# Optimization experiments

Hardware: AMD Instinct MI355X
Metric: run time of the kernel (lower is better)

Reference implementation:

```python
import jax, jax.numpy as jnp
import numpy as np

N = 20000
NEG_SLOPE = 0.2


def gatv2_layer(x, src, dst, edge_attr, Wl, bl, Wr, br, We, att, bias, H, C):
    """PyG GATv2Conv: add self-loops (edge_attr fill='mean'), gather-score-softmax-aggregate."""
    n = x.shape[0]
    E = src.shape[0]
    # --- add self loops, self-loop edge_attr = mean of incoming edge_attr per node ---
    ea_sum = jax.ops.segment_sum(edge_attr, dst, num_segments=n)
    deg = jax.ops.segment_sum(jnp.ones((E, 1), x.dtype), dst, num_segments=n)
    ea_loop = ea_sum / jnp.maximum(deg, 1.0)
    loop = jnp.arange(n)
    src_a = jnp.concatenate([src, loop])
    dst_a = jnp.concatenate([dst, loop])
    ea = jnp.concatenate([edge_attr, ea_loop], axis=0)
    # --- linear projections ---
    xl = (x @ Wl + bl).reshape(n, H, C)   # source-side features
    xr = (x @ Wr + br).reshape(n, H, C)   # target-side features
    e = (ea @ We).reshape(-1, H, C)       # edge features
    # --- per-edge GATv2 attention score ---
    m = xl[src_a] + xr[dst_a] + e                          # [E', H, C]
    s = jnp.sum(jax.nn.leaky_relu(m, NEG_SLOPE) * att, -1)  # [E', H]
    # --- softmax over incoming edges of each target node ---
    smax = jax.ops.segment_max(s, dst_a, num_segments=n)
    ex = jnp.exp(s - smax[dst_a])
    denom = jax.ops.segment_sum(ex, dst_a, num_segments=n)
    alpha = ex / (denom[dst_a] + 1e-16)                    # [E', H]
    # --- aggregate messages (alpha * x_l[src]) ---
    out = jax.ops.segment_sum(alpha[..., None] * xl[src_a], dst_a, num_segments=n)
    return out.reshape(n, H * C) + bias


def setup_inputs() -> dict:
    key = jax.random.key(0)
    ks = jax.random.split(key, 20)
    F, HID, H1, A = 128, 32, 8, 128
    E = 640000
    d = {}
    d["x"] = jax.random.normal(ks[0], (N, F), jnp.float32)
    d["edge_index"] = jax.random.randint(ks[1], (2, E), 0, N, jnp.int32).astype(jnp.int64)
    d["edge_attr"] = jax.random.normal(ks[2], (E, 1), jnp.float32)
    # layer 1 params (in=F, out=HID, heads=H1)
    d["W1l"] = jax.random.normal(ks[3], (F, H1 * HID), jnp.float32) * 0.05
    d["b1l"] = jnp.zeros((H1 * HID,), jnp.float32)
    d["W1r"] = jax.random.normal(ks[4], (F, H1 * HID), jnp.float32) * 0.05
    d["b1r"] = jnp.zeros((H1 * HID,), jnp.float32)
    d["We1"] = jax.random.normal(ks[5], (1, H1 * HID), jnp.float32) * 0.05
    d["att1"] = jax.random.normal(ks[6], (H1, HID), jnp.float32) * 0.05
    d["bias1"] = jnp.zeros((H1 * HID,), jnp.float32)
    # layer 2 params (in=H1*HID, out=A, heads=1)
    d["W2l"] = jax.random.normal(ks[7], (H1 * HID, A), jnp.float32) * 0.05
    d["b2l"] = jnp.zeros((A,), jnp.float32)
    d["W2r"] = jax.random.normal(ks[8], (H1 * HID, A), jnp.float32) * 0.05
    d["b2r"] = jnp.zeros((A,), jnp.float32)
    d["We2"] = jax.random.normal(ks[9], (1, A), jnp.float32) * 0.05
    d["att2"] = jax.random.normal(ks[10], (1, A), jnp.float32) * 0.05
    d["bias2"] = jnp.zeros((A,), jnp.float32)
    d["alpha"] = jnp.array(0.0, jnp.float32)
    return d


def reference(x, edge_index, edge_attr, W1l, b1l, W1r, b1r, We1, att1, bias1,
              W2l, b2l, W2r, b2r, We2, att2, bias2, alpha):
    src, dst = edge_index[0], edge_index[1]
    h = jax.nn.relu(gatv2_layer(x, src, dst, edge_attr, W1l, b1l, W1r, b1r,
                                We1, att1, bias1, H=8, C=32))
    h = jax.nn.relu(gatv2_layer(h, src, dst, edge_attr, W2l, b2l, W2r, b2r,
                                We2, att2, bias2, H=1, C=128))
    pooled = jnp.mean(h, axis=0, keepdims=True)  # global_mean_pool, single graph -> [1, A]
    return jax.nn.softmax(pooled, axis=1), jax.nn.sigmoid(alpha)
```

## Files before the change

### kernel.cpp

```cpp
#include <hip/hip_runtime.h>
#include <math.h>

#define NEG_SLOPE 0.2f
#define LOG2E 1.4426950408889634f

typedef __attribute__((ext_vector_type(8))) short short8;
typedef __attribute__((ext_vector_type(4))) float f32x4;
typedef __attribute__((ext_vector_type(2))) float v2f;

__device__ __forceinline__ int imin(int a, int b) { return a < b ? a : b; }

__device__ __forceinline__ unsigned int f2bf(float f) {
    unsigned int u = __float_as_uint(f);
    return (u + 0x7fffu + ((u >> 16) & 1u)) >> 16;
}
__device__ __forceinline__ float fast_exp2(float x) {
#if __has_builtin(__builtin_amdgcn_exp2f)
    return __builtin_amdgcn_exp2f(x);
#else
    return exp2f(x);
#endif
}
__device__ __forceinline__ unsigned char f2fp8(float v) {
    return (unsigned char)(__builtin_amdgcn_cvt_pk_fp8_f32(v, v, 0, false) & 0xff);
}
template <int CTRL>
__device__ __forceinline__ float dpp_add(float v) {
    int t = __builtin_amdgcn_update_dpp(0, __float_as_int(v), CTRL, 0xF, 0xF, true);
    return v + __int_as_float(t);
}
__device__ __forceinline__ v2f pk_fma(v2f a, v2f b, v2f c) {
    v2f d;
    asm("v_pk_fma_f32 %0, %1, %2, %3" : "=v"(d) : "v"(a), "v"(b), "v"(c));
    return d;
}
__device__ __forceinline__ v2f pk_add(v2f a, v2f b) {
    v2f d;
    asm("v_pk_add_f32 %0, %1, %2" : "=v"(d) : "v"(a), "v"(b));
    return d;
}

__global__ void fused_prep(const int* __restrict__ ei, const float* __restrict__ ea,
                           unsigned long long* __restrict__ hist, int E,
                           const float* __restrict__ x, unsigned short* __restrict__ xb, int nF4,
                           const float* __restrict__ W1l, const float* __restrict__ W1r,
                           const float* __restrict__ W2l, const float* __restrict__ W2r,
                           const float* __restrict__ b1l, const float* __restrict__ b1r,
                           const float* __restrict__ b2l, const float* __restrict__ b2r,
                           unsigned short* __restrict__ Wt1, unsigned short* __restrict__ Wt2,
                           float* __restrict__ b1cat, float* __restrict__ b2cat,
                           int F, int HC1, int HC2) {
    int i = blockIdx.x * blockDim.x + threadIdx.x;
    if (i < E) {
        int d = ei[E + i];
        long long fx = (long long)__float2int_rn(ea[i] * 65536.0f);
        unsigned long long v = ((unsigned long long)fx << 32) | 1ull;
        atomicAdd(&hist[(size_t)d * 8], v);
        return;
    }
    int j = i - E;
    if (j < nF4) {
        float4 v = ((const float4*)x)[j];
        uint2 r;
        r.x = f2bf(v.x) | (f2bf(v.y) << 16);
        r.y = f2bf(v.z) | (f2bf(v.w) << 16);
        ((uint2*)xb)[j] = r;
        return;
    }
    int k = j - nF4;
    int S1 = F * HC1, S2 = HC1 * HC2;
    if (k < S1) {
        int kk = k / HC1, nn = k - kk * HC1;
        Wt1[(size_t)nn * F + kk] = (unsigned short)f2bf(W1l[k]);
    } else if (k < 2 * S1) {
        int m = k - S1;
        int kk = m / HC1, nn = m - kk * HC1;
        Wt1[(size_t)(HC1 + nn) * F + kk] = (unsigned short)f2bf(W1r[m]);
    } else if (k < 2 * S1 + S2) {
        int m = k - 2 * S1;
        int kk = m / HC2, nn = m - kk * HC2;
        Wt2[(size_t)nn * HC1 + kk] = (unsigned short)f2bf(W2l[m]);
    } else if (k < 2 * S1 + 2 * S2) {
        int m = k - 2 * S1 - S2;
        int kk = m / HC2, nn = m - kk * HC2;
        Wt2[(size_t)(HC2 + nn) * HC1 + kk] = (unsigned short)f2bf(W2r[m]);
    } else if (k < 2 * S1 + 2 * S2 + 2 * HC1) {
        int m = k - 2 * S1 - 2 * S2;
        b1cat[m] = (m < HC1) ? b1l[m] : b1r[m - HC1];
    } else if (k < 2 * S1 + 2 * S2 + 2 * HC1 + 2 * HC2) {
        int m = k - 2 * S1 - 2 * S2 - 2 * HC1;
        b2cat[m] = (m < HC2) ? b2l[m] : b2r[m - HC2];
    }
}

__global__ void scan_a(const unsigned long long* __restrict__ hist, int* __restrict__ bsum, int n) {
    __shared__ int wred[4];
    int base = blockIdx.x * 1024;
    int tid = threadIdx.x;
    int s = 0;
#pragma unroll
    for (int k = 0; k < 4; ++k) {
        int i = base + tid + k * 256;
        if (i < n) s += (int)(hist[(size_t)i * 8] & 0xffffffffull);
    }
#pragma unroll
    for (int off = 32; off > 0; off >>= 1) s += __shfl_xor(s, off, 64);
    if ((tid & 63) == 0) wred[tid >> 6] = s;
    __syncthreads();
    if (tid == 0) bsum[blockIdx.x] = wred[0] + wred[1] + wred[2] + wred[3];
}

__global__ void scan_c(const unsigned long long* __restrict__ hist,
                       const int* __restrict__ bsum, int* __restrict__ row_ptr,
                       int* __restrict__ wptr_pad, float* __restrict__ ea_loop,
                       int n, int B) {
    __shared__ int wtot[4];
    __shared__ int sh_base;
    int tid = threadIdx.x;
    int wid = tid >> 6, lane = tid & 63;
    int i0 = blockIdx.x * 1024 + tid * 4;
    int dcnt[4]; float esum[4];
#pragma unroll
    for (int k = 0; k < 4; ++k) {
        if (i0 + k < n) {
            unsigned long long h = hist[(size_t)(i0 + k) * 8];
            dcnt[k] = (int)(h & 0xffffffffull);
            esum[k] = (float)((int)(h >> 32)) * (1.0f / 65536.0f);
        } else { dcnt[k] = 0; esum[k] = 0.0f; }
    }
    int tsum = dcnt[0] + dcnt[1] + dcnt[2] + dcnt[3];
    int s = tsum;
#pragma unroll
    for (int off = 1; off < 64; off <<= 1) {
        int t = __shfl_up(s, off, 64);
        if (lane >= off) s += t;
    }
    if (lane == 63) wtot[wid] = s;
    if (tid < 64) {
        int v   = (tid < B) ? bsum[tid] : 0;
        int pre = (tid < (int)blockIdx.x) ? v : 0;
        int tot = v;
#pragma unroll
        for (int off = 32; off > 0; off >>= 1) {
            pre += __shfl_xor(pre, off, 64);
            tot += __shfl_xor(tot, off, 64);
        }
        if (tid == 0) {
            sh_base = pre;
            if (blockIdx.x == 0) row_ptr[n] = tot;
        }
    }
    __syncthreads();
    int wpre = 0;
#pragma unroll
    for (int k = 0; k < 4; ++k) if (k < wid) wpre += wtot[k];
    int pre = sh_base + wpre + (s - tsum);
    if (i0 < n) {
        int4 e;
        e.x = pre;
        e.y = pre + dcnt[0];
        e.z = e.y + dcnt[1];
        e.w = e.z + dcnt[2];
        *(int4*)(row_ptr + i0) = e;
        int ev[4] = { e.x, e.y, e.z, e.w };
        float4 el;
        el.x = esum[0] / fmaxf((float)dcnt[0], 1.0f);
        el.y = esum[1] / fmaxf((float)dcnt[1], 1.0f);
        el.z = esum[2] / fmaxf((float)dcnt[2], 1.0f);
        el.w = esum[3] / fmaxf((float)dcnt[3], 1.0f);
        *(float4*)(ea_loop + i0) = el;
#pragma unroll
        for (int k = 0; k < 4; ++k) wptr_pad[(size_t)(i0 + k) * 16] = ev[k];
    }
}

__global__ void edge_scatter(const int* __restrict__ ei, const float* __restrict__ ea,
                             int* __restrict__ wptr_pad, int2* __restrict__ spk, int E) {
    int e = blockIdx.x * blockDim.x + threadIdx.x;
    if (e < E) {
        int d = ei[E + e];
        int pos = atomicAdd(&wptr_pad[(size_t)d * 16], 1);
        spk[pos] = make_int2(ei[e], __float_as_int(ea[e]));
    }
}

template <bool OUT_FP8>
__global__ void __launch_bounds__(256)
gemm_bf16(const unsigned short* __restrict__ A, const unsigned short* __restrict__ Bt,
          const float* __restrict__ bias, void* __restrict__ Cv,
          int M, int N, int K) {
    __shared__ __attribute__((aligned(16))) unsigned short As[64 * 40];
    __shared__ __attribute__((aligned(16))) unsigned short Bs[64 * 40];
    int tid  = threadIdx.x;
    int wave = tid >> 6, lane = tid & 63;
    int m0 = blockIdx.x * 64, n0 = blockIdx.y * 64;
    int row = tid >> 2, kg = (tid & 3) * 8;

    f32x4 acc[4] = {};
    for (int kk = 0; kk < K; kk += 32) {
        int gm = m0 + row;
        uint4 av;
        if (gm < M) av = *(const uint4*)(A + (size_t)gm * K + kk + kg);
        else        av = make_uint4(0, 0, 0, 0);
        *(uint4*)&As[row * 40 + kg] = av;
        uint4 bv = *(const uint4*)(Bt + (size_t)(n0 + row) * K + kk + kg);
        *(uint4*)&Bs[row * 40 + kg] = bv;
        __syncthreads();
        short8 a = *(const short8*)&As[(wave * 16 + (lane & 15)) * 40 + (lane >> 4) * 8];
#pragma unroll
        for (int g = 0; g < 4; ++g) {
            short8 b = *(const short8*)&Bs[(g * 16 + (lane & 15)) * 40 + (lane >> 4) * 8];
            acc[g] = __builtin_amdgcn_mfma_f32_16x16x32_bf16(a, b, acc[g], 0, 0, 0);
        }
        __syncthreads();
    }
#pragma unroll
    for (int g = 0; g < 4; ++g) {
        int col = n0 + g * 16 + (lane & 15);
        float bs = bias[col];
#pragma unroll
        for (int r = 0; r < 4; ++r) {
            int grow = m0 + wave * 16 + (lane >> 4) * 4 + r;
            if (grow < M) {
                float val = acc[g][r] + bs;
                if constexpr (OUT_FP8) {
                    ((unsigned char*)Cv)[(size_t)grow * N + col] = f2fp8(val);
                } else {
                    ((unsigned short*)Cv)[(size_t)grow * N + col] = (unsigned short)f2bf(val);
                }
            }
        }
    }
}

template <int NG>
__device__ __forceinline__ void unp2(uint2 u, v2f* xf) {
    xf[0] = __builtin_amdgcn_cvt_pk_f32_fp8(u.x, false);
    xf[1] = __builtin_amdgcn_cvt_pk_f32_fp8(u.x, true);
    if constexpr (NG == 4) {
        xf[2] = __builtin_amdgcn_cvt_pk_f32_fp8(u.y, false);
        xf[3] = __builtin_amdgcn_cvt_pk_f32_fp8(u.y, true);
    }
}
template <int G>
__device__ __forceinline__ float grp_reduce32(float vs) {
    vs = dpp_add<0xB1>(vs);
    if constexpr (G >= 4)  vs = dpp_add<0x4E>(vs);
    if constexpr (G >= 8)  vs = dpp_add<0x141>(vs);
    if constexpr (G >= 16) vs = dpp_add<0x140>(vs);
    if constexpr (G >= 32) {
        int t = __builtin_amdgcn_ds_swizzle(__float_as_int(vs), 0x401F);
        vs += __int_as_float(t);
    }
    return vs;
}

template <int HC, int STRIDE, int C, int OUT_MODE>
__global__ void __launch_bounds__(256)
gat_agg(const unsigned char* __restrict__ xlr,
        const float* __restrict__ We, const float* __restrict__ att,
        const float* __restrict__ bias,
        const int* __restrict__ row_ptr, const int2* __restrict__ spk,
        const float* __restrict__ ea_loop,
        void* __restrict__ out, int n) {
    constexpr int NV = HC / 32;
    constexpr int NG = NV / 2;
    constexpr int G  = C / NV;
    constexpr int SHIFT = (STRIDE == 512) ? 9 : 8;
    constexpr float K23 = 2.0f / 3.0f;
    int wave = threadIdx.x >> 6;
    int lane = threadIdx.x & 63;
    int node = blockIdx.x * 4 + wave;
    if (node >= n) return;
    unsigned int lo32 = (unsigned int)(lane & 31) * NV;
    int half = lane >> 5;

    auto ldd = [&](unsigned int off) -> uint2 {
        uint2 r;
        if constexpr (NV == 8) r = *(const uint2*)(xlr + off);
        else { r.x = *(const unsigned int*)(xlr + off); r.y = 0u; }
        return r;
    };
    auto gat = [&](int s) -> uint2 {
        return ldd(((unsigned int)s << SHIFT) + lo32);
    };

    v2f xr2[NG], We2[NG], att62[NG], o2[NG];
    unp2<NG>(ldd(((unsigned int)node << SHIFT) + HC + lo32), xr2);
#pragma unroll
    for (int g = 0; g < NG; ++g) {
        We2[g]   = *(const v2f*)(We  + lo32 + 2 * g);
        v2f a    = *(const v2f*)(att + lo32 + 2 * g);
        att62[g] = a * (0.6f * LOG2E);
        o2[g]    = v2f{0.0f, 0.0f};
    }
    float l = 0.0f;

    int start = __builtin_amdgcn_readfirstlane(row_ptr[node]);
    int end   = __builtin_amdgcn_readfirstlane(row_ptr[node + 1]);
    float ea_l = ea_loop[node];

    auto process = [&](uint2 du, float w, bool maskhi) {
        v2f xf[NG];
        unp2<NG>(du, xf);
        v2f w2 = {w, w};
        v2f vs6 = {0.0f, 0.0f};
        float vs4 = 0.0f;
#pragma unroll
        for (int g = 0; g < NG; ++g) {
            v2f t  = pk_fma(w2, We2[g], xr2[g]);
            v2f mm = pk_add(xf[g], t);
            vs6 = pk_fma(att62[g], mm, vs6);
            vs4 = fmaf(fabsf(mm.x), att62[g].x, vs4);
            vs4 = fmaf(fabsf(mm.y), att62[g].y, vs4);
        }
        float vs = fmaf(K23, vs4, vs6.x + vs6.y);
        vs = grp_reduce32<G>(vs);
        float pr = fast_exp2(vs);
        if (maskhi && lane >= 32) pr = 0.0f;
        l += pr;
        v2f pr2 = {pr, pr};
#pragma unroll
        for (int g = 0; g < NG; ++g) o2[g] = pk_fma(xf[g], pr2, o2[g]);
    };

    process(ldd(((unsigned int)node << SHIFT) + lo32), ea_l, true);

    int cnt = end - start;
    int npair = cnt >> 1;
    const int2* pp = spk + start + half;

    if (npair >= 2) {
        int2 sA = pp[0], sB = pp[2];
        uint2 gA = gat(sA.x);
        int p = 0;
        for (; p + 2 < npair; p += 2) {
            uint2 gB = gat(sB.x);
            int2 sC = pp[2 * p + 4];
            process(gA, __int_as_float(sA.y), false);
            uint2 gC = gat(sC.x);
            int2 sD = pp[2 * p + 6];
            process(gB, __int_as_float(sB.y), false);
            sA = sC; sB = sD; gA = gC;
        }
        if (npair - p == 2) {
            uint2 gB = gat(sB.x);
            process(gA, __int_as_float(sA.y), false);
            process(gB, __int_as_float(sB.y), false);
        } else {
            process(gA, __int_as_float(sA.y), false);
        }
    } else if (npair == 1) {
        int2 sA = pp[0];
        process(gat(sA.x), __int_as_float(sA.y), false);
    }
    if (cnt & 1) {
        int2 st = spk[end - 1];
        process(gat(st.x), __int_as_float(st.y), true);
    }

    l += __shfl_xor(l, 32, 64);
#pragma unroll
    for (int g = 0; g < NG; ++g) {
        o2[g].x += __shfl_xor(o2[g].x, 32, 64);
        o2[g].y += __shfl_xor(o2[g].y, 32, 64);
    }
    float inv = 1.0f / (l + 1e-16f);

    if (lane < 32) {
        float v[NV];
#pragma unroll
        for (int g = 0; g < NG; ++g) {
            v2f b = *(const v2f*)(bias + lo32 + 2 * g);
            v[2 * g]     = fmaxf(o2[g].x * inv + b.x, 0.0f);
            v[2 * g + 1] = fmaxf(o2[g].y * inv + b.y, 0.0f);
        }
        if constexpr (OUT_MODE == 0) {
            unsigned short* op = (unsigned short*)out + (size_t)node * HC + lo32;
            if constexpr (NV == 8) {
                uint4 t;
                t.x = f2bf(v[0]) | (f2bf(v[1]) << 16);
                t.y = f2bf(v[2]) | (f2bf(v[3]) << 16);
                t.z = f2bf(v[4]) | (f2bf(v[5]) << 16);
                t.w = f2bf(v[6]) | (f2bf(v[7]) << 16);
                *(uint4*)op = t;
            } else {
                uint2 t;
                t.x = f2bf(v[0]) | (f2bf(v[1]) << 16);
                t.y = f2bf(v[2]) | (f2bf(v[3]) << 16);
                *(uint2*)op = t;
            }
        } else {
            float* pacc = (float*)out + (size_t)(blockIdx.x & 255) * 128 + lo32;
#pragma unroll
            for (int j = 0; j < NV; ++j) atomicAdd(&pacc[j], v[j]);
        }
    }
}

__global__ void __launch_bounds__(1024)
pool_final(const float* __restrict__ partial, int nb,
           const float* __restrict__ alpha_in,
           float* __restrict__ out, int n) {
    __shared__ float acc[8][128];
    __shared__ float red[4];
    int t = threadIdx.x & 127;
    int g = threadIdx.x >> 7;
    float s = 0.0f;
    for (int b = g; b < nb; b += 8) s += partial[b * 128 + t];
    acc[g][t] = s;
    __syncthreads();
    if (threadIdx.x < 128) {
        float tot = 0.0f;
#pragma unroll
        for (int k = 0; k < 8; ++k) tot += acc[k][t];
        float mean = tot / (float)n;
        float mx = mean;
#pragma unroll
        for (int off = 32; off > 0; off >>= 1) mx = fmaxf(mx, __shfl_xor(mx, off, 64));
        if ((t & 63) == 0) red[t >> 6] = mx;
        __syncthreads();
        mx = fmaxf(red[0], red[1]);
        float ex = __expf(mean - mx);
        float sm = ex;
#pragma unroll
        for (int off = 32; off > 0; off >>= 1) sm += __shfl_xor(sm, off, 64);
        if ((t & 63) == 0) red[2 + (t >> 6)] = sm;
        __syncthreads();
        sm = red[2] + red[3];
        out[t] = ex / sm;
        if (t == 0) out[128] = 1.0f / (1.0f + __expf(-alpha_in[0]));
    }
}

extern "C" void kernel_launch(void* const* d_in, const int* in_sizes, int n_in,
                              void* d_out, int out_size, void* d_ws, size_t ws_size,
                              hipStream_t stream) {
    const float* x    = (const float*)d_in[0];
    const int*   ei   = (const int*)d_in[1];
    const float* ea   = (const float*)d_in[2];
    const float* W1l  = (const float*)d_in[3];
    const float* b1l  = (const float*)d_in[4];
    const float* W1r  = (const float*)d_in[5];
    const float* b1r  = (const float*)d_in[6];
    const float* We1  = (const float*)d_in[7];
    const float* att1 = (const float*)d_in[8];
    const float* bias1= (const float*)d_in[9];
    const float* W2l  = (const float*)d_in[10];
    const float* b2l  = (const float*)d_in[11];
    const float* W2r  = (const float*)d_in[12];
    const float* b2r  = (const float*)d_in[13];
    const float* We2  = (const float*)d_in[14];
    const float* att2 = (const float*)d_in[15];
    const float* bias2= (const float*)d_in[16];
    const float* alpha= (const float*)d_in[17];
    float* out = (float*)d_out;

    const int F = 128, HC1 = 256, HC2 = 128;
    const int n = in_sizes[0] / F;
    const int E = in_sizes[1] / 2;
    const int B = (n + 1023) / 1024;

    char* ws = (char*)d_ws;
    size_t off = 0;
    auto alloc = [&](size_t bytes) { size_t p = off; off += (bytes + 255) & ~(size_t)255; return p; };

    unsigned long long* hist = (unsigned long long*)(ws + alloc((size_t)n * 8 * 8));
    int*   row_ptr = (int*)  (ws + alloc((size_t)(n + 1) * 4));
    int*   wptr    = (int*)  (ws + alloc((size_t)n * 16 * 4));
    float* ea_loop = (float*)(ws + alloc((size_t)n * 4));
    int*   bsum    = (int*)  (ws + alloc(64 * 4));
    int2*  spk     = (int2*) (ws + alloc((size_t)(E + 8) * 8));
    unsigned short* xb   = (unsigned short*)(ws + alloc((size_t)n * F * 2));
    unsigned short* Wt1  = (unsigned short*)(ws + alloc((size_t)F * (2 * HC1) * 2));
    unsigned short* Wt2  = (unsigned short*)(ws + alloc((size_t)HC1 * (2 * HC2) * 2));
    float* b1cat   = (float*)(ws + alloc((size_t)2 * HC1 * 4));
    float* b2cat   = (float*)(ws + alloc((size_t)2 * HC2 * 4));
    unsigned char* xlr1 = (unsigned char*)(ws + alloc((size_t)n * 2 * HC1));
    unsigned short* h1  = (unsigned short*)(ws + alloc((size_t)n * HC1 * 2));
    float* partial = (float*)(ws + alloc((size_t)256 * 128 * 4));
    unsigned char* xlr2 = xlr1;
    const int NB_SLOTS = 256;

    (void)hipMemsetAsync(hist, 0, (size_t)n * 8 * 8, stream);
    (void)hipMemsetAsync(partial, 0, (size_t)NB_SLOTS * 128 * 4, stream);
    (void)hipMemsetAsync(spk + E, 0, 8 * sizeof(int2), stream);

    int tb = 256;
    {
        int nF4  = n * F / 4;
        int WTOT = 2 * F * HC1 + 2 * HC1 * HC2 + 2 * HC1 + 2 * HC2;
        int total = E + nF4 + WTOT;
        fused_prep<<<(total + tb - 1) / tb, tb, 0, stream>>>(
            ei, ea, hist, E, x, xb, nF4,
            W1l, W1r, W2l, W2r, b1l, b1r, b2l, b2r,
            Wt1, Wt2, b1cat, b2cat, F, HC1, HC2);
    }
    scan_a<<<B, 256, 0, stream>>>(hist, bsum, n);
    scan_c<<<B, 256, 0, stream>>>(hist, bsum, row_ptr, wptr, ea_loop, n, B);
    edge_scatter<<<(E + tb - 1) / tb, tb, 0, stream>>>(ei, ea, wptr, spk, E);

    {
        dim3 grid((n + 63) / 64, (2 * HC1) / 64);
        gemm_bf16<true><<<grid, 256, 0, stream>>>(xb, Wt1, b1cat, xlr1, n, 2 * HC1, F);
    }
    gat_agg<256, 512, 32, 0><<<(n + 3) / 4, 256, 0, stream>>>(
        xlr1, We1, att1, bias1, row_ptr, spk, ea_loop, h1, n);

    {
        dim3 grid((n + 63) / 64, (2 * HC2) / 64);
        gemm_bf16<true><<<grid, 256, 0, stream>>>(h1, Wt2, b2cat, xlr2, n, 2 * HC2, HC1);
    }
    gat_agg<128, 256, 128, 1><<<(n + 3) / 4, 256, 0, stream>>>(
        xlr2, We2, att2, bias2, row_ptr, spk, ea_loop, partial, n);

    pool_final<<<1, 1024, 0, stream>>>(partial, NB_SLOTS, alpha, out, n);
}
```

Baseline: 284.1 us.

## Deepen gather prefetch to eight edges and block-reduce pooled output before atomics

The edge loop in the aggregation kernel now keeps eight neighbour gathers in flight, two groups of four issued ahead of use, instead of two. Nodes with fewer than eight edge pairs fall back to a simple loop. This is meant to hide more gather latency. In the pooling mode the four waves of a block first sum their outputs in shared memory, so only one wave issues atomics, cutting global atomic traffic by four. The padding at the end of the edge buffer and its memset are removed. The deeper prefetch raises register pressure, and the new barrier requires inactive waves to stay in the kernel.

```diff
diff --git a/kernel.cpp b/kernel.cpp
--- a/kernel.cpp
+++ b/kernel.cpp
@@ -268,132 +268,162 @@
     constexpr int G  = C / NV;
     constexpr int SHIFT = (STRIDE == 512) ? 9 : 8;
     constexpr float K23 = 2.0f / 3.0f;
+    __shared__ float red[4][128];
     int wave = threadIdx.x >> 6;
     int lane = threadIdx.x & 63;
     int node = blockIdx.x * 4 + wave;
-    if (node >= n) return;
+    bool active = node < n;
+    if (OUT_MODE == 0 && !active) return;
     unsigned int lo32 = (unsigned int)(lane & 31) * NV;
     int half = lane >> 5;
 
-    auto ldd = [&](unsigned int off) -> uint2 {
-        uint2 r;
-        if constexpr (NV == 8) r = *(const uint2*)(xlr + off);
-        else { r.x = *(const unsigned int*)(xlr + off); r.y = 0u; }
-        return r;
-    };
-    auto gat = [&](int s) -> uint2 {
-        return ldd(((unsigned int)s << SHIFT) + lo32);
-    };
-
-    v2f xr2[NG], We2[NG], att62[NG], o2[NG];
-    unp2<NG>(ldd(((unsigned int)node << SHIFT) + HC + lo32), xr2);
-#pragma unroll
-    for (int g = 0; g < NG; ++g) {
-        We2[g]   = *(const v2f*)(We  + lo32 + 2 * g);
-        v2f a    = *(const v2f*)(att + lo32 + 2 * g);
-        att62[g] = a * (0.6f * LOG2E);
-        o2[g]    = v2f{0.0f, 0.0f};
-    }
-    float l = 0.0f;
-
-    int start = __builtin_amdgcn_readfirstlane(row_ptr[node]);
-    int end   = __builtin_amdgcn_readfirstlane(row_ptr[node + 1]);
-    float ea_l = ea_loop[node];
-
-    auto process = [&](uint2 du, float w, bool maskhi) {
-        v2f xf[NG];
-        unp2<NG>(du, xf);
-        v2f w2 = {w, w};
-        v2f vs6 = {0.0f, 0.0f};
-        float vs4 = 0.0f;
+    float vout[NV];
+#pragma unroll
+    for (int j = 0; j < NV; ++j) vout[j] = 0.0f;
+
+    if (active) {
+        auto ldd = [&](unsigned int off) -> uint2 {
+            uint2 r;
+            if constexpr (NV == 8) r = *(const uint2*)(xlr + off);
+            else { r.x = *(const unsigned int*)(xlr + off); r.y = 0u; }
+            return r;
+        };
+        auto gat = [&](int s) -> uint2 {
+            return ldd(((unsigned int)s << SHIFT) + lo32);
+        };
+
+        v2f xr2[NG], We2[NG], att62[NG], o2[NG];
+        unp2<NG>(ldd(((unsigned int)node << SHIFT) + HC + lo32), xr2);
 #pragma unroll
         for (int g = 0; g < NG; ++g) {
-            v2f t  = pk_fma(w2, We2[g], xr2[g]);
-            v2f mm = pk_add(xf[g], t);
-            vs6 = pk_fma(att62[g], mm, vs6);
-            vs4 = fmaf(fabsf(mm.x), att62[g].x, vs4);
-            vs4 = fmaf(fabsf(mm.y), att62[g].y, vs4);
-        }
-        float vs = fmaf(K23, vs4, vs6.x + vs6.y);
-        vs = grp_reduce32<G>(vs);
-        float pr = fast_exp2(vs);
-        if (maskhi && lane >= 32) pr = 0.0f;
-        l += pr;
-        v2f pr2 = {pr, pr};
-#pragma unroll
-        for (int g = 0; g < NG; ++g) o2[g] = pk_fma(xf[g], pr2, o2[g]);
-    };
-
-    process(ldd(((unsigned int)node << SHIFT) + lo32), ea_l, true);
-
-    int cnt = end - start;
-    int npair = cnt >> 1;
-    const int2* pp = spk + start + half;
-
-    if (npair >= 2) {
-        int2 sA = pp[0], sB = pp[2];
-        uint2 gA = gat(sA.x);
-        int p = 0;
-        for (; p + 2 < npair; p += 2) {
-            uint2 gB = gat(sB.x);
-            int2 sC = pp[2 * p + 4];
-            process(gA, __int_as_float(sA.y), false);
-            uint2 gC = gat(sC.x);
-            int2 sD = pp[2 * p + 6];
-            process(gB, __int_as_float(sB.y), false);
-            sA = sC; sB = sD; gA = gC;
-        }
-        if (npair - p == 2) {
-            uint2 gB = gat(sB.x);
-            process(gA, __int_as_float(sA.y), false);
-            process(gB, __int_as_float(sB.y), false);
+            We2[g]   = *(const v2f*)(We  + lo32 + 2 * g);
+            v2f a    = *(const v2f*)(att + lo32 + 2 * g);
+            att62[g] = a * (0.6f * LOG2E);
+            o2[g]    = v2f{0.0f, 0.0f};
+        }
+        float l = 0.0f;
+
+        int start = __builtin_amdgcn_readfirstlane(row_ptr[node]);
+        int end   = __builtin_amdgcn_readfirstlane(row_ptr[node + 1]);
+        float ea_l = ea_loop[node];
+
+        auto process = [&](uint2 du, float w, bool maskhi) {
+            v2f xf[NG];
+            unp2<NG>(du, xf);
+            v2f w2 = {w, w};
+            v2f vs6 = {0.0f, 0.0f};
+            float vs4 = 0.0f;
+#pragma unroll
+            for (int g = 0; g < NG; ++g) {
+                v2f t  = pk_fma(w2, We2[g], xr2[g]);
+                v2f mm = pk_add(xf[g], t);
+                vs6 = pk_fma(att62[g], mm, vs6);
+                vs4 = fmaf(fabsf(mm.x), att62[g].x, vs4);
+                vs4 = fmaf(fabsf(mm.y), att62[g].y, vs4);
+            }
+            float vs = fmaf(K23, vs4, vs6.x + vs6.y);
+            vs = grp_reduce32<G>(vs);
+            float pr = fast_exp2(vs);
+            if (maskhi && lane >= 32) pr = 0.0f;
+            l += pr;
+            v2f pr2 = {pr, pr};
+#pragma unroll
+            for (int g = 0; g < NG; ++g) o2[g] = pk_fma(xf[g], pr2, o2[g]);
+        };
+        auto W = [&](int2 s) -> float { return __int_as_float(s.y); };
+
+        process(ldd(((unsigned int)node << SHIFT) + lo32), ea_l, true);
+
+        int cnt = end - start;
+        int npair = cnt >> 1;
+        const int2* pp = spk + start + half;
+
+        if (npair >= 8) {
+            int2 s0 = pp[0],  s1 = pp[2],  s2 = pp[4],  s3 = pp[6];
+            int2 s4 = pp[8],  s5 = pp[10], s6 = pp[12], s7 = pp[14];
+            uint2 g0 = gat(s0.x), g1 = gat(s1.x), g2 = gat(s2.x), g3 = gat(s3.x);
+            int p = 0;
+            for (; p + 16 <= npair; p += 8) {
+                uint2 h0 = gat(s4.x), h1 = gat(s5.x), h2 = gat(s6.x), h3 = gat(s7.x);
+                float w0 = W(s0), w1 = W(s1), w2 = W(s2), w3 = W(s3);
+                s0 = pp[2*(p+8)];  s1 = pp[2*(p+9)];
+                s2 = pp[2*(p+10)]; s3 = pp[2*(p+11)];
+                process(g0, w0, false); process(g1, w1, false);
+                process(g2, w2, false); process(g3, w3, false);
+                g0 = gat(s0.x); g1 = gat(s1.x); g2 = gat(s2.x); g3 = gat(s3.x);
+                float w4 = W(s4), w5 = W(s5), w6 = W(s6), w7 = W(s7);
+                s4 = pp[2*(p+12)]; s5 = pp[2*(p+13)];
+                s6 = pp[2*(p+14)]; s7 = pp[2*(p+15)];
+                process(h0, w4, false); process(h1, w5, false);
+                process(h2, w6, false); process(h3, w7, false);
+            }
+            uint2 h0 = gat(s4.x), h1 = gat(s5.x), h2 = gat(s6.x), h3 = gat(s7.x);
+            process(g0, W(s0), false); process(g1, W(s1), false);
+            process(g2, W(s2), false); process(g3, W(s3), false);
+            process(h0, W(s4), false); process(h1, W(s5), false);
+            process(h2, W(s6), false); process(h3, W(s7), false);
+            for (int k = p + 8; k < npair; ++k) {
+                int2 t = pp[2 * k];
+                process(gat(t.x), W(t), false);
+            }
         } else {
-            process(gA, __int_as_float(sA.y), false);
-        }
-    } else if (npair == 1) {
-        int2 sA = pp[0];
-        process(gat(sA.x), __int_as_float(sA.y), false);
-    }
-    if (cnt & 1) {
-        int2 st = spk[end - 1];
-        process(gat(st.x), __int_as_float(st.y), true);
-    }
-
-    l += __shfl_xor(l, 32, 64);
-#pragma unroll
-    for (int g = 0; g < NG; ++g) {
-        o2[g].x += __shfl_xor(o2[g].x, 32, 64);
-        o2[g].y += __shfl_xor(o2[g].y, 32, 64);
-    }
-    float inv = 1.0f / (l + 1e-16f);
-
-    if (lane < 32) {
-        float v[NV];
+            for (int k = 0; k < npair; ++k) {
+                int2 t = pp[2 * k];
+                process(gat(t.x), W(t), false);
+            }
+        }
+        if (cnt & 1) {
+            int2 st = spk[end - 1];
+            process(gat(st.x), W(st), true);
+        }
+
+        l += __shfl_xor(l, 32, 64);
 #pragma unroll
         for (int g = 0; g < NG; ++g) {
-            v2f b = *(const v2f*)(bias + lo32 + 2 * g);
-            v[2 * g]     = fmaxf(o2[g].x * inv + b.x, 0.0f);
-            v[2 * g + 1] = fmaxf(o2[g].y * inv + b.y, 0.0f);
-        }
-        if constexpr (OUT_MODE == 0) {
-            unsigned short* op = (unsigned short*)out + (size_t)node * HC + lo32;
-            if constexpr (NV == 8) {
-                uint4 t;
-                t.x = f2bf(v[0]) | (f2bf(v[1]) << 16);
-                t.y = f2bf(v[2]) | (f2bf(v[3]) << 16);
-                t.z = f2bf(v[4]) | (f2bf(v[5]) << 16);
-                t.w = f2bf(v[6]) | (f2bf(v[7]) << 16);
-                *(uint4*)op = t;
-            } else {
-                uint2 t;
-                t.x = f2bf(v[0]) | (f2bf(v[1]) << 16);
-                t.y = f2bf(v[2]) | (f2bf(v[3]) << 16);
-                *(uint2*)op = t;
-            }
-        } else {
-            float* pacc = (float*)out + (size_t)(blockIdx.x & 255) * 128 + lo32;
-#pragma unroll
-            for (int j = 0; j < NV; ++j) atomicAdd(&pacc[j], v[j]);
+            o2[g].x += __shfl_xor(o2[g].x, 32, 64);
+            o2[g].y += __shfl_xor(o2[g].y, 32, 64);
+        }
+        float inv = 1.0f / (l + 1e-16f);
+
+        if (lane < 32) {
+#pragma unroll
+            for (int g = 0; g < NG; ++g) {
+                v2f b = *(const v2f*)(bias + lo32 + 2 * g);
+                vout[2 * g]     = fmaxf(o2[g].x * inv + b.x, 0.0f);
+                vout[2 * g + 1] = fmaxf(o2[g].y * inv + b.y, 0.0f);
+            }
+            if constexpr (OUT_MODE == 0) {
+                unsigned short* op = (unsigned short*)out + (size_t)node * HC + lo32;
+                if constexpr (NV == 8) {
+                    uint4 t;
+                    t.x = f2bf(vout[0]) | (f2bf(vout[1]) << 16);
+                    t.y = f2bf(vout[2]) | (f2bf(vout[3]) << 16);
+                    t.z = f2bf(vout[4]) | (f2bf(vout[5]) << 16);
+                    t.w = f2bf(vout[6]) | (f2bf(vout[7]) << 16);
+                    *(uint4*)op = t;
+                } else {
+                    uint2 t;
+                    t.x = f2bf(vout[0]) | (f2bf(vout[1]) << 16);
+                    t.y = f2bf(vout[2]) | (f2bf(vout[3]) << 16);
+                    *(uint2*)op = t;
+                }
+            }
+        }
+    }
+
+    if constexpr (OUT_MODE == 1) {
+        if (lane < 32) {
+#pragma unroll
+            for (int j = 0; j < NV; ++j) red[wave][lo32 + j] = vout[j];
+        }
+        __syncthreads();
+        if (wave == 0) {
+            int c = lane;
+            float a = red[0][c] + red[1][c] + red[2][c] + red[3][c];
+            float b = red[0][c + 64] + red[1][c + 64] + red[2][c + 64] + red[3][c + 64];
+            float* pacc = (float*)out + (size_t)(blockIdx.x & 255) * 128;
+            atomicAdd(&pacc[c], a);
+            atomicAdd(&pacc[c + 64], b);
         }
     }
 }
@@ -470,7 +500,7 @@
     int*   wptr    = (int*)  (ws + alloc((size_t)n * 16 * 4));
     float* ea_loop = (float*)(ws + alloc((size_t)n * 4));
     int*   bsum    = (int*)  (ws + alloc(64 * 4));
-    int2*  spk     = (int2*) (ws + alloc((size_t)(E + 8) * 8));
+    int2*  spk     = (int2*) (ws + alloc((size_t)E * 8));
     unsigned short* xb   = (unsigned short*)(ws + alloc((size_t)n * F * 2));
     unsigned short* Wt1  = (unsigned short*)(ws + alloc((size_t)F * (2 * HC1) * 2));
     unsigned short* Wt2  = (unsigned short*)(ws + alloc((size_t)HC1 * (2 * HC2) * 2));
@@ -484,7 +514,6 @@
 
     (void)hipMemsetAsync(hist, 0, (size_t)n * 8 * 8, stream);
     (void)hipMemsetAsync(partial, 0, (size_t)NB_SLOTS * 128 * 4, stream);
-    (void)hipMemsetAsync(spk + E, 0, 8 * sizeof(int2), stream);
 
     int tb = 256;
     {
```

New measurement: 279.1 us. About the same (-1.7%).
